# Optimization experiments

Hardware: AMD Instinct MI355X
Metric: run time of the kernel (lower is better)

The kernel has to match this reference:

```python
import jax, jax.numpy as jnp
import numpy as np

B, N, D, K = 8, 2048, 512, 16


def setup_inputs() -> dict:
    key = jax.random.key(0)
    k1, k2, k3, k4, k5 = jax.random.split(key, 5)
    s = 1.0 / np.sqrt(D)
    return {
        "x": jax.random.normal(k1, (B, N, D), dtype=jnp.float32),
        "attn_w": jax.random.uniform(k2, (K, D), jnp.float32, -s, s),
        "attn_b": jax.random.uniform(k3, (K,), jnp.float32, -s, s),
        "w_merged": jax.random.uniform(k4, (D, D), jnp.float32, -s, s),
        "w_orig": jax.random.uniform(k5, (D, D), jnp.float32, -s, s),
    }


def reference(x, attn_w, attn_b, w_merged, w_orig):
    b, n, d = x.shape
    k = attn_w.shape[0]
    # cosine similarity matrix [B,N,N]
    xn = x / jnp.linalg.norm(x, axis=2, keepdims=True)
    w = jnp.einsum('bnd,bmd->bnm', xn, xn)
    # top-k neighbours per row
    _, idx = jax.lax.top_k(w, k)  # [B,N,K]
    bi = jnp.arange(b)[:, None, None]
    ni = jnp.arange(n)[None, :, None]
    # scatter 1s at top-k positions, then symmetrize (mutual-knn mask)
    mask = jnp.zeros((b, n, n), x.dtype).at[bi, ni, idx].set(1.0)
    mask = mask * jnp.swapaxes(mask, 1, 2)
    # learned per-neighbour attention logits scattered into dense [B,N,N]
    attn = x @ attn_w.T + attn_b  # [B,N,K]
    attn_full = jnp.zeros((b, n, n), x.dtype).at[bi, ni, idx].set(attn)
    scores = attn_full * mask + (-1e9) * (1.0 - mask)
    adj = jax.nn.softmax(scores, axis=2)
    # weighted aggregation + two projections
    merged = jnp.einsum('bnm,bmd->bnd', adj, x)
    out = jax.nn.relu(merged @ w_merged.T) + x @ w_orig.T
    return out
```

## Files before the change

kernel.cpp:

```cpp
#include <hip/hip_runtime.h>
#include <math.h>


#define NTOK 2048
#define DIM 512

typedef __attribute__((ext_vector_type(8))) __bf16 bf16x8;
typedef __attribute__((ext_vector_type(4))) float f32x4;
typedef __attribute__((ext_vector_type(8))) unsigned short ushort8;

#define GLDS(gp, lp)                                                      \
  __builtin_amdgcn_global_load_lds(                                       \
      (const __attribute__((address_space(1))) void*)(gp),                \
      (__attribute__((address_space(3))) void*)(lp), 16, 0, 0)

__device__ __forceinline__ ushort f2b(float f) {
  unsigned u = __float_as_uint(f);
  return (ushort)((u + 0x7fffu + ((u >> 16) & 1u)) >> 16);
}
__device__ __forceinline__ float b2f(ushort h) {
  return __uint_as_float((unsigned)h << 16);
}
__device__ __forceinline__ ushort f2key(float v) {
  union { _Float16 h; ushort u; } cv;
  cv.h = (_Float16)v;
  ushort hb = cv.u;
  return (hb & 0x8000u) ? (ushort)~hb : (ushort)(hb | 0x8000u);
}

__global__ __launch_bounds__(64) void k_norm(const float* __restrict__ x,
                                             const float* __restrict__ aw,
                                             const float* __restrict__ ab,
                                             ushort* __restrict__ xnb,
                                             ushort* __restrict__ xb,
                                             double* __restrict__ inv64,
                                             float* __restrict__ L) {
  int row = blockIdx.x, lane = threadIdx.x;
  const float* xr = x + (size_t)row * DIM;
  float4 a = *(const float4*)&xr[lane * 8];
  float4 b = *(const float4*)&xr[lane * 8 + 4];

  float s[16];
#pragma unroll
  for (int k = 0; k < 16; ++k) {
    const float4 w0 = *(const float4*)&aw[(size_t)k * DIM + lane * 8];
    const float4 w1 = *(const float4*)&aw[(size_t)k * DIM + lane * 8 + 4];
    s[k] = a.x * w0.x + a.y * w0.y + a.z * w0.z + a.w * w0.w + b.x * w1.x +
           b.y * w1.y + b.z * w1.z + b.w * w1.w;
  }
#pragma unroll
  for (int off = 1; off < 64; off <<= 1)
#pragma unroll
    for (int k = 0; k < 16; ++k) s[k] += __shfl_xor(s[k], off);

  double ss = (double)a.x * a.x + (double)a.y * a.y + (double)a.z * a.z +
              (double)a.w * a.w + (double)b.x * b.x + (double)b.y * b.y +
              (double)b.z * b.z + (double)b.w * b.w;
#pragma unroll
  for (int off = 32; off >= 1; off >>= 1) ss += __shfl_xor(ss, off);
  double inv = 1.0 / sqrt(ss);
  if (lane == 0) {
    inv64[row] = inv;
#pragma unroll
    for (int k = 0; k < 16; ++k) L[(size_t)row * 16 + k] = s[k] + ab[k];
  }
  float f = (float)inv;
  size_t o = (size_t)row * DIM + lane * 8;
  ushort4 r0 = {f2b(a.x), f2b(a.y), f2b(a.z), f2b(a.w)};
  ushort4 r1 = {f2b(b.x), f2b(b.y), f2b(b.z), f2b(b.w)};
  *(ushort4*)&xb[o] = r0;
  *(ushort4*)&xb[o + 4] = r1;
  ushort4 n0 = {f2b(a.x * f), f2b(a.y * f), f2b(a.z * f), f2b(a.w * f)};
  ushort4 n1 = {f2b(b.x * f), f2b(b.y * f), f2b(b.z * f), f2b(b.w * f)};
  *(ushort4*)&xnb[o] = n0;
  *(ushort4*)&xnb[o + 4] = n1;
}

__global__ __launch_bounds__(256) void k_castw(const float* __restrict__ a,
                                               const float* __restrict__ b,
                                               ushort* __restrict__ ab,
                                               ushort* __restrict__ bb) {
  int i = (blockIdx.x * 256 + threadIdx.x) * 4;
  float4 va = *(const float4*)&a[i];
  float4 vb = *(const float4*)&b[i];
  ushort4 oa = {f2b(va.x), f2b(va.y), f2b(va.z), f2b(va.w)};
  ushort4 ob = {f2b(vb.x), f2b(vb.y), f2b(vb.z), f2b(vb.w)};
  *(ushort4*)&ab[i] = oa;
  *(ushort4*)&bb[i] = ob;
}

__device__ __forceinline__ void stage2(const ushort* __restrict__ A,
                                       const ushort* __restrict__ B,
                                       ushort* lA, ushort* lB, int rb, int cb,
                                       int kt, int wv, int ln) {
#pragma unroll
  for (int j = 0; j < 2; ++j) {
    int c = j * 256 + wv * 64 + ln;
    int r = c >> 2, seg = c & 3;
    GLDS(A + (size_t)(rb + r) * DIM + kt + seg * 8, lA + c * 8);
    GLDS(B + (size_t)(cb + r) * DIM + kt + seg * 8, lB + c * 8);
  }
}

__device__ __forceinline__ void frag_mfma(const ushort* lA, const ushort* lB,
                                          int wm, int wn, int col, int quad,
                                          f32x4 (&acc)[4][4]) {
  bf16x8 af[4], bf[4];
#pragma unroll
  for (int i = 0; i < 4; ++i) {
    af[i] = *(const bf16x8*)&lA[(wm * 64 + i * 16 + col) * 32 + quad * 8];
    bf[i] = *(const bf16x8*)&lB[(wn * 64 + i * 16 + col) * 32 + quad * 8];
  }
#pragma unroll
  for (int i = 0; i < 4; ++i)
#pragma unroll
    for (int j = 0; j < 4; ++j)
      acc[i][j] =
          __builtin_amdgcn_mfma_f32_16x16x32_bf16(af[i], bf[j], acc[i][j], 0, 0, 0);
}

__global__ __launch_bounds__(256) void k_simgemm(const ushort* __restrict__ Xn,
                                                 ushort* __restrict__ Skey) {
  __shared__ __align__(16) ushort lA0[128 * 32];
  __shared__ __align__(16) ushort lB0[128 * 32];
  __shared__ __align__(16) ushort st[128 * 136];
  ushort* lA1 = st;
  ushort* lB1 = st + 128 * 32;
  int tid = threadIdx.x;
  int z = blockIdx.z;
  const ushort* Xb = Xn + (size_t)z * NTOK * DIM;
  ushort* Sb = Skey + (size_t)z * NTOK * NTOK;
  int ti = 0, rem = blockIdx.x;
  while (rem >= 16 - ti) { rem -= 16 - ti; ++ti; }
  int tj = ti + rem;
  int rb = ti * 128, cb = tj * 128;
  int wv = tid >> 6, ln = tid & 63;
  int wm = wv >> 1, wn = wv & 1;
  int col = ln & 15, quad = ln >> 4;
  f32x4 zero = {0.f, 0.f, 0.f, 0.f};
  f32x4 acc[4][4];
#pragma unroll
  for (int i = 0; i < 4; ++i)
#pragma unroll
    for (int j = 0; j < 4; ++j) acc[i][j] = zero;

  stage2(Xb, Xb, lA0, lB0, rb, cb, 0, wv, ln);
  __syncthreads();
#pragma unroll
  for (int kt16 = 0; kt16 < 16; ++kt16) {
    const ushort* cA = (kt16 & 1) ? lA1 : lA0;
    const ushort* cB = (kt16 & 1) ? lB1 : lB0;
    if (kt16 < 15)
      stage2(Xb, Xb, (kt16 & 1) ? lA0 : lA1, (kt16 & 1) ? lB0 : lB1, rb, cb,
             (kt16 + 1) * 32, wv, ln);
    frag_mfma(cA, cB, wm, wn, col, quad, acc);
    __syncthreads();
  }

#pragma unroll
  for (int i = 0; i < 4; ++i)
#pragma unroll
    for (int j = 0; j < 4; ++j) {
      int r0 = wm * 64 + i * 16 + quad * 4;
      int c = wn * 64 + j * 16 + col;
      ushort4 kk = {f2key(acc[i][j][0]), f2key(acc[i][j][1]),
                    f2key(acc[i][j][2]), f2key(acc[i][j][3])};
      *(ushort4*)&Sb[(size_t)(cb + c) * NTOK + rb + r0] = kk;
      st[(r0 + 0) * 136 + c] = kk.x;
      st[(r0 + 1) * 136 + c] = kk.y;
      st[(r0 + 2) * 136 + c] = kk.z;
      st[(r0 + 3) * 136 + c] = kk.w;
    }
  __syncthreads();
#pragma unroll
  for (int p = 0; p < 8; ++p) {
    int r = p * 16 + (tid >> 4);
    int cs = (tid & 15) * 8;
    ushort8 row = *(const ushort8*)&st[r * 136 + cs];
    *(ushort8*)&Sb[(size_t)(rb + r) * NTOK + cb + cs] = row;
  }
}

__global__ __launch_bounds__(256) void k_proj(const ushort* __restrict__ Mg,
                                              const ushort* __restrict__ Wm,
                                              const ushort* __restrict__ Xg,
                                              const ushort* __restrict__ Wo,
                                              float* __restrict__ out) {
  __shared__ __align__(16) ushort lds[32768];
  ushort* A1a = lds;
  ushort* B1a = lds + 4096;
  ushort* A2a = lds + 8192;
  ushort* B2a = lds + 12288;
  ushort* A1b = lds + 16384;
  ushort* B1b = lds + 20480;
  ushort* A2b = lds + 24576;
  ushort* B2b = lds + 28672;
  int tid = threadIdx.x;
  int rb = blockIdx.x * 128, cb = blockIdx.y * 128;
  int wv = tid >> 6, ln = tid & 63;
  int wm = wv >> 1, wn = wv & 1;
  int col = ln & 15, quad = ln >> 4;
  f32x4 zero = {0.f, 0.f, 0.f, 0.f};
  f32x4 a1[4][4], a2[4][4];
#pragma unroll
  for (int i = 0; i < 4; ++i)
#pragma unroll
    for (int j = 0; j < 4; ++j) { a1[i][j] = zero; a2[i][j] = zero; }

  stage2(Mg, Wm, A1a, B1a, rb, cb, 0, wv, ln);
  stage2(Xg, Wo, A2a, B2a, rb, cb, 0, wv, ln);
  __syncthreads();
#pragma unroll
  for (int kt16 = 0; kt16 < 16; ++kt16) {
    const bool odd = kt16 & 1;
    const ushort* cA1 = odd ? A1b : A1a;
    const ushort* cB1 = odd ? B1b : B1a;
    const ushort* cA2 = odd ? A2b : A2a;
    const ushort* cB2 = odd ? B2b : B2a;
    if (kt16 < 15) {
      stage2(Mg, Wm, odd ? A1a : A1b, odd ? B1a : B1b, rb, cb,
             (kt16 + 1) * 32, wv, ln);
      stage2(Xg, Wo, odd ? A2a : A2b, odd ? B2a : B2b, rb, cb,
             (kt16 + 1) * 32, wv, ln);
    }
    frag_mfma(cA1, cB1, wm, wn, col, quad, a1);
    frag_mfma(cA2, cB2, wm, wn, col, quad, a2);
    __syncthreads();
  }

#pragma unroll
  for (int i = 0; i < 4; ++i)
#pragma unroll
    for (int j = 0; j < 4; ++j)
#pragma unroll
      for (int r = 0; r < 4; ++r) {
        int m = rb + wm * 64 + i * 16 + quad * 4 + r;
        int n = cb + wn * 64 + j * 16 + col;
        out[(size_t)m * DIM + n] = fmaxf(a1[i][j][r], 0.f) + a2[i][j][r];
      }
}

#define TARGET 24

__device__ __forceinline__ void scan_pick(const unsigned* hist, int lane,
                                          int tgt, int* out_v,
                                          unsigned* out_cntv1) {
  int base = lane * 4;
  unsigned h0 = hist[0 * 256 + base + 0] + hist[1 * 256 + base + 0] +
                hist[2 * 256 + base + 0] + hist[3 * 256 + base + 0];
  unsigned h1 = hist[0 * 256 + base + 1] + hist[1 * 256 + base + 1] +
                hist[2 * 256 + base + 1] + hist[3 * 256 + base + 1];
  unsigned h2 = hist[0 * 256 + base + 2] + hist[1 * 256 + base + 2] +
                hist[2 * 256 + base + 2] + hist[3 * 256 + base + 2];
  unsigned h3 = hist[0 * 256 + base + 3] + hist[1 * 256 + base + 3] +
                hist[2 * 256 + base + 3] + hist[3 * 256 + base + 3];
  unsigned s3 = h3, s2 = h2 + s3, s1 = h1 + s2, s0 = h0 + s1;
  unsigned inc = s0;
#pragma unroll
  for (int off = 1; off < 64; off <<= 1) {
    unsigned o = __shfl_down(inc, off);
    if (lane + off < 64) inc += o;
  }
  unsigned above = inc - s0;
  int vb = -1;
  if (above + s0 >= (unsigned)tgt) vb = base + 0;
  if (above + s1 >= (unsigned)tgt) vb = base + 1;
  if (above + s2 >= (unsigned)tgt) vb = base + 2;
  if (above + s3 >= (unsigned)tgt) vb = base + 3;
  int v = vb;
#pragma unroll
  for (int off = 1; off < 64; off <<= 1) v = max(v, __shfl_xor(v, off));
  unsigned v1 = 0;
  if ((v >> 2) == lane) {
    int k = v & 3;
    v1 = (k == 0) ? above + s1 : (k == 1) ? above + s2
                               : (k == 2) ? above + s3 : above;
  }
  v1 = __shfl(v1, v >> 2);
  *out_v = v;
  *out_cntv1 = v1;
}

__global__ __launch_bounds__(256) void k_topk(const ushort* __restrict__ simk,
                                              const float* __restrict__ x,
                                              const double* __restrict__ inv64,
                                              int* __restrict__ idx16,
                                              int batch0, int pbm1, int pbsh) {
  int zi = blockIdx.x & pbm1;
  int n = blockIdx.x >> pbsh;
  int batch = batch0 + zi;
  int t = threadIdx.x;
  int wave = t >> 6, lane = t & 63;
  __shared__ unsigned hist[4 * 256];
  __shared__ int lidx[32];
  __shared__ double vals[32];
  __shared__ int shv, sneed, sthr, lcnt;
  const ushort* srow = simk + ((size_t)zi * NTOK + (size_t)n) * NTOK;

  const float* xrow = x + ((size_t)batch * NTOK + n) * DIM;
  float4 xa0 = *(const float4*)&xrow[lane * 8];
  float4 xa1 = *(const float4*)&xrow[lane * 8 + 4];
  double dinvn = inv64[(size_t)batch * NTOK + n];

  ushort kv[8];
  {
    ushort8 v8 = *(const ushort8*)&srow[t * 8];
#pragma unroll
    for (int e = 0; e < 8; ++e) kv[e] = v8[e];
  }
#pragma unroll
  for (int i = 0; i < 4; ++i) hist[t + 256 * i] = 0;
  if (t == 0) lcnt = 0;
  __syncthreads();
#pragma unroll
  for (int j = 0; j < 8; ++j)
    atomicAdd(&hist[wave * 256 + (kv[j] >> 8)], 1u);
  __syncthreads();
  if (wave == 0) {
    int v;
    unsigned v1;
    scan_pick(hist, lane, TARGET, &v, &v1);
    if (lane == 0) { shv = v; sneed = TARGET - (int)v1; }
  }
  __syncthreads();
  int v = shv;
#pragma unroll
  for (int i = 0; i < 4; ++i) hist[t + 256 * i] = 0;
  __syncthreads();
#pragma unroll
  for (int j = 0; j < 8; ++j)
    if ((kv[j] >> 8) == v) atomicAdd(&hist[wave * 256 + (kv[j] & 255)], 1u);
  __syncthreads();
  if (wave == 0) {
    int u;
    unsigned dummy;
    scan_pick(hist, lane, sneed, &u, &dummy);
    if (lane == 0) sthr = (v << 8) | u;
  }
  __syncthreads();
  unsigned thr = (unsigned)sthr;
#pragma unroll
  for (int j = 0; j < 8; ++j) {
    if ((unsigned)kv[j] >= thr) {
      int slot = atomicAdd(&lcnt, 1);
      if (slot < 32) lidx[slot] = t * 8 + j;
    }
  }
  __syncthreads();
  int c = lcnt < 32 ? lcnt : 32;
  for (int s = wave; s < c; s += 4) {
    int m = lidx[s];
    const float* xc = x + ((size_t)batch * NTOK + m) * DIM;
    float4 b0 = *(const float4*)&xc[lane * 8];
    float4 b1 = *(const float4*)&xc[lane * 8 + 4];
    double sacc = 0.0;
    sacc = fma((double)xa0.x, (double)b0.x, sacc);
    sacc = fma((double)xa0.y, (double)b0.y, sacc);
    sacc = fma((double)xa0.z, (double)b0.z, sacc);
    sacc = fma((double)xa0.w, (double)b0.w, sacc);
    sacc = fma((double)xa1.x, (double)b1.x, sacc);
    sacc = fma((double)xa1.y, (double)b1.y, sacc);
    sacc = fma((double)xa1.z, (double)b1.z, sacc);
    sacc = fma((double)xa1.w, (double)b1.w, sacc);
#pragma unroll
    for (int off = 1; off < 64; off <<= 1) sacc += __shfl_xor(sacc, off);
    if (lane == 0)
      vals[s] = sacc * dinvn * inv64[(size_t)batch * NTOK + m];
  }
  __syncthreads();
  if (t < 32) {
    double sv = (t < c) ? vals[t] : -1.0e300;
    int si = (t < c) ? lidx[t] : 0x7FFFFFFF;
#pragma unroll
    for (int k = 2; k <= 32; k <<= 1) {
#pragma unroll
      for (int jj = k >> 1; jj > 0; jj >>= 1) {
        double ov = __shfl_xor(sv, jj);
        int oi = __shfl_xor(si, jj);
        bool lower = (t & jj) == 0;
        bool desc = (t & k) == 0;
        bool takeFirst = (lower == desc);
        bool otherFirst = (ov > sv) || (ov == sv && oi < si);
        if (takeFirst == otherFirst) { sv = ov; si = oi; }
      }
    }
    if (t < 16) idx16[((size_t)batch * NTOK + n) * 16 + t] = si;
  }
}

__global__ __launch_bounds__(128) void k_merge(const ushort* __restrict__ xb,
                                               const int* __restrict__ idx16,
                                               const float* __restrict__ L,
                                               ushort* __restrict__ mergedb) {
  int b = blockIdx.x & 7;
  int n = blockIdx.x >> 3;
  int row = (b << 11) | n;
  int t = threadIdx.x;
  __shared__ float ps[16];
  __shared__ int ms[16];
  if (t < 64) {
    int k = t & 15;
    int m = idx16[(size_t)row * 16 + k];
    const int* mrow = idx16 + (size_t)(b * NTOK + m) * 16;
    int4 q0 = *(const int4*)&mrow[0];
    int4 q1 = *(const int4*)&mrow[4];
    int4 q2 = *(const int4*)&mrow[8];
    int4 q3 = *(const int4*)&mrow[12];
    bool mut = (q0.x == n) | (q0.y == n) | (q0.z == n) | (q0.w == n) |
               (q1.x == n) | (q1.y == n) | (q1.z == n) | (q1.w == n) |
               (q2.x == n) | (q2.y == n) | (q2.z == n) | (q2.w == n) |
               (q3.x == n) | (q3.y == n) | (q3.z == n) | (q3.w == n);
    float l = mut ? L[(size_t)row * 16 + k] : -__builtin_inff();
    float mx = l;
#pragma unroll
    for (int off = 1; off < 16; off <<= 1) mx = fmaxf(mx, __shfl_xor(mx, off));
    float e = mut ? __expf(l - mx) : 0.0f;
    float den = e;
#pragma unroll
    for (int off = 1; off < 16; off <<= 1) den += __shfl_xor(den, off);
    if (t < 16) { ps[t] = e / den; ms[t] = m; }
  }
  __syncthreads();
  float4 acc = {0.f, 0.f, 0.f, 0.f};
#pragma unroll
  for (int k = 0; k < 16; ++k) {
    float pk = ps[k];
    if (pk != 0.0f) {
      ushort4 v = *(const ushort4*)&xb[(size_t)(b * NTOK + ms[k]) * DIM + t * 4];
      acc.x = fmaf(pk, b2f(v.x), acc.x);
      acc.y = fmaf(pk, b2f(v.y), acc.y);
      acc.z = fmaf(pk, b2f(v.z), acc.z);
      acc.w = fmaf(pk, b2f(v.w), acc.w);
    }
  }
  ushort4 o = {f2b(acc.x), f2b(acc.y), f2b(acc.z), f2b(acc.w)};
  *(ushort4*)&mergedb[(size_t)row * DIM + t * 4] = o;
}

extern "C" void kernel_launch(void* const* d_in, const int* in_sizes, int n_in,
                              void* d_out, int out_size, void* d_ws,
                              size_t ws_size, hipStream_t stream) {
  const float* x = (const float*)d_in[0];
  const float* attn_w = (const float*)d_in[1];
  const float* attn_b = (const float*)d_in[2];
  const float* w_merged = (const float*)d_in[3];
  const float* w_orig = (const float*)d_in[4];
  float* out = (float*)d_out;

  char* w = (char*)d_ws;
  ushort* xnb = (ushort*)(w);
  ushort* xb = (ushort*)(w + 16777216);
  double* inv64 = (double*)(w + 33554432);
  ushort* wmb = (ushort*)(w + 33685504);
  ushort* wob = (ushort*)(w + 34209792);
  int* idx16 = (int*)(w + 34734080);
  float* L = (float*)(w + 35782656);
  ushort* simk = (ushort*)(w + 36831232);
  ushort* mergedb = (ushort*)(w + 36831232);

  size_t fixed = 36831232ull, per = 8388608ull;
  int pb = 1, pbsh = 0;
  if (ws_size >= fixed + 8 * per) { pb = 8; pbsh = 3; }
  else if (ws_size >= fixed + 4 * per) { pb = 4; pbsh = 2; }
  else if (ws_size >= fixed + 2 * per) { pb = 2; pbsh = 1; }

  k_norm<<<16384, 64, 0, stream>>>(x, attn_w, attn_b, xnb, xb, inv64, L);
  k_castw<<<256, 256, 0, stream>>>(w_merged, w_orig, wmb, wob);
  for (int b = 0; b < 8; b += pb) {
    k_simgemm<<<dim3(136, 1, pb), 256, 0, stream>>>(
        xnb + (size_t)b * NTOK * DIM, simk);
    k_topk<<<NTOK * pb, 256, 0, stream>>>(simk, x, inv64, idx16, b, pb - 1,
                                          pbsh);
  }
  k_merge<<<16384, 128, 0, stream>>>(xb, idx16, L, mergedb);
  k_proj<<<dim3(128, 4), 256, 0, stream>>>(mergedb, wmb, xb, wob, out);
}
```

Baseline: 301.1 us.

## Run top-k selection with one wavefront per row, dropping block barriers

Rewrites the per-row top-k kernel to use a single 64-lane wavefront instead of four. Each lane now holds 32 keys, builds one shared histogram instead of four per-wave ones, and replaces the atomic candidate compaction with a ballot/popcount prefix. This removes the __syncthreads barriers and the cross-wave histogram reduction. In exchange each row gets less parallelism, the exact rescoring loop runs serially on one wave, and the code relies on wave-synchronous LDS ordering with no explicit barriers.

```diff
diff --git a/kernel.cpp b/kernel.cpp
--- a/kernel.cpp
+++ b/kernel.cpp
@@ -245,16 +245,8 @@
 __device__ __forceinline__ void scan_pick(const unsigned* hist, int lane,
                                           int tgt, int* out_v,
                                           unsigned* out_cntv1) {
-  int base = lane * 4;
-  unsigned h0 = hist[0 * 256 + base + 0] + hist[1 * 256 + base + 0] +
-                hist[2 * 256 + base + 0] + hist[3 * 256 + base + 0];
-  unsigned h1 = hist[0 * 256 + base + 1] + hist[1 * 256 + base + 1] +
-                hist[2 * 256 + base + 1] + hist[3 * 256 + base + 1];
-  unsigned h2 = hist[0 * 256 + base + 2] + hist[1 * 256 + base + 2] +
-                hist[2 * 256 + base + 2] + hist[3 * 256 + base + 2];
-  unsigned h3 = hist[0 * 256 + base + 3] + hist[1 * 256 + base + 3] +
-                hist[2 * 256 + base + 3] + hist[3 * 256 + base + 3];
-  unsigned s3 = h3, s2 = h2 + s3, s1 = h1 + s2, s0 = h0 + s1;
+  uint4 h = *(const uint4*)&hist[lane * 4];
+  unsigned s3 = h.w, s2 = h.z + s3, s1 = h.y + s2, s0 = h.x + s1;
   unsigned inc = s0;
 #pragma unroll
   for (int off = 1; off < 64; off <<= 1) {
@@ -262,6 +254,7 @@
     if (lane + off < 64) inc += o;
   }
   unsigned above = inc - s0;
+  int base = lane * 4;
   int vb = -1;
   if (above + s0 >= (unsigned)tgt) vb = base + 0;
   if (above + s1 >= (unsigned)tgt) vb = base + 1;
@@ -281,74 +274,68 @@
   *out_cntv1 = v1;
 }
 
-__global__ __launch_bounds__(256) void k_topk(const ushort* __restrict__ simk,
-                                              const float* __restrict__ x,
-                                              const double* __restrict__ inv64,
-                                              int* __restrict__ idx16,
-                                              int batch0, int pbm1, int pbsh) {
+__global__ __launch_bounds__(64) void k_topk(const ushort* __restrict__ simk,
+                                             const float* __restrict__ x,
+                                             const double* __restrict__ inv64,
+                                             int* __restrict__ idx16,
+                                             int batch0, int pbm1, int pbsh) {
   int zi = blockIdx.x & pbm1;
   int n = blockIdx.x >> pbsh;
   int batch = batch0 + zi;
-  int t = threadIdx.x;
-  int wave = t >> 6, lane = t & 63;
-  __shared__ unsigned hist[4 * 256];
+  int lane = threadIdx.x;
+  __shared__ __align__(16) unsigned hist1[256];
+  __shared__ __align__(16) unsigned hist2[256];
   __shared__ int lidx[32];
   __shared__ double vals[32];
-  __shared__ int shv, sneed, sthr, lcnt;
   const ushort* srow = simk + ((size_t)zi * NTOK + (size_t)n) * NTOK;
-
   const float* xrow = x + ((size_t)batch * NTOK + n) * DIM;
+
   float4 xa0 = *(const float4*)&xrow[lane * 8];
   float4 xa1 = *(const float4*)&xrow[lane * 8 + 4];
   double dinvn = inv64[(size_t)batch * NTOK + n];
 
-  ushort kv[8];
-  {
-    ushort8 v8 = *(const ushort8*)&srow[t * 8];
-#pragma unroll
-    for (int e = 0; e < 8; ++e) kv[e] = v8[e];
-  }
-#pragma unroll
-  for (int i = 0; i < 4; ++i) hist[t + 256 * i] = 0;
-  if (t == 0) lcnt = 0;
-  __syncthreads();
-#pragma unroll
-  for (int j = 0; j < 8; ++j)
-    atomicAdd(&hist[wave * 256 + (kv[j] >> 8)], 1u);
-  __syncthreads();
-  if (wave == 0) {
-    int v;
-    unsigned v1;
-    scan_pick(hist, lane, TARGET, &v, &v1);
-    if (lane == 0) { shv = v; sneed = TARGET - (int)v1; }
-  }
-  __syncthreads();
-  int v = shv;
-#pragma unroll
-  for (int i = 0; i < 4; ++i) hist[t + 256 * i] = 0;
-  __syncthreads();
-#pragma unroll
-  for (int j = 0; j < 8; ++j)
-    if ((kv[j] >> 8) == v) atomicAdd(&hist[wave * 256 + (kv[j] & 255)], 1u);
-  __syncthreads();
-  if (wave == 0) {
-    int u;
-    unsigned dummy;
-    scan_pick(hist, lane, sneed, &u, &dummy);
-    if (lane == 0) sthr = (v << 8) | u;
-  }
-  __syncthreads();
-  unsigned thr = (unsigned)sthr;
-#pragma unroll
-  for (int j = 0; j < 8; ++j) {
-    if ((unsigned)kv[j] >= thr) {
-      int slot = atomicAdd(&lcnt, 1);
-      if (slot < 32) lidx[slot] = t * 8 + j;
+  ushort8 kk[4];
+#pragma unroll
+  for (int r = 0; r < 4; ++r)
+    kk[r] = *(const ushort8*)&srow[(r * 64 + lane) * 8];
+  hist1[lane] = 0; hist1[lane + 64] = 0;
+  hist1[lane + 128] = 0; hist1[lane + 192] = 0;
+  hist2[lane] = 0; hist2[lane + 64] = 0;
+  hist2[lane + 128] = 0; hist2[lane + 192] = 0;
+#pragma unroll
+  for (int r = 0; r < 4; ++r)
+#pragma unroll
+    for (int j = 0; j < 8; ++j)
+      atomicAdd(&hist1[kk[r][j] >> 8], 1u);
+  int v;
+  unsigned v1;
+  scan_pick(hist1, lane, TARGET, &v, &v1);
+  int need = TARGET - (int)v1;
+#pragma unroll
+  for (int r = 0; r < 4; ++r)
+#pragma unroll
+    for (int j = 0; j < 8; ++j)
+      if ((kk[r][j] >> 8) == v) atomicAdd(&hist2[kk[r][j] & 255], 1u);
+  int u;
+  unsigned dummy;
+  scan_pick(hist2, lane, need, &u, &dummy);
+  unsigned thr = (unsigned)((v << 8) | u);
+  int cnt = 0;
+  unsigned long long ltmask = (1ull << lane) - 1ull;
+#pragma unroll
+  for (int r = 0; r < 4; ++r)
+#pragma unroll
+    for (int j = 0; j < 8; ++j) {
+      bool p = (unsigned)kk[r][j] >= thr;
+      unsigned long long m = __ballot(p);
+      if (p) {
+        int pos = cnt + __popcll(m & ltmask);
+        if (pos < 32) lidx[pos] = (r * 64 + lane) * 8 + j;
+      }
+      cnt += __popcll(m);
     }
-  }
-  __syncthreads();
-  int c = lcnt < 32 ? lcnt : 32;
-  for (int s = wave; s < c; s += 4) {
+  int c = cnt < 32 ? cnt : 32;
+  for (int s = 0; s < c; ++s) {
     int m = lidx[s];
     const float* xc = x + ((size_t)batch * NTOK + m) * DIM;
     float4 b0 = *(const float4*)&xc[lane * 8];
@@ -367,24 +354,23 @@
     if (lane == 0)
       vals[s] = sacc * dinvn * inv64[(size_t)batch * NTOK + m];
   }
-  __syncthreads();
-  if (t < 32) {
-    double sv = (t < c) ? vals[t] : -1.0e300;
-    int si = (t < c) ? lidx[t] : 0x7FFFFFFF;
+  if (lane < 32) {
+    double sv = (lane < c) ? vals[lane] : -1.0e300;
+    int si = (lane < c) ? lidx[lane] : 0x7FFFFFFF;
 #pragma unroll
     for (int k = 2; k <= 32; k <<= 1) {
 #pragma unroll
       for (int jj = k >> 1; jj > 0; jj >>= 1) {
         double ov = __shfl_xor(sv, jj);
         int oi = __shfl_xor(si, jj);
-        bool lower = (t & jj) == 0;
-        bool desc = (t & k) == 0;
+        bool lower = (lane & jj) == 0;
+        bool desc = (lane & k) == 0;
         bool takeFirst = (lower == desc);
         bool otherFirst = (ov > sv) || (ov == sv && oi < si);
         if (takeFirst == otherFirst) { sv = ov; si = oi; }
       }
     }
-    if (t < 16) idx16[((size_t)batch * NTOK + n) * 16 + t] = si;
+    if (lane < 16) idx16[((size_t)batch * NTOK + n) * 16 + lane] = si;
   }
 }
 
@@ -469,8 +455,8 @@
   for (int b = 0; b < 8; b += pb) {
     k_simgemm<<<dim3(136, 1, pb), 256, 0, stream>>>(
         xnb + (size_t)b * NTOK * DIM, simk);
-    k_topk<<<NTOK * pb, 256, 0, stream>>>(simk, x, inv64, idx16, b, pb - 1,
-                                          pbsh);
+    k_topk<<<NTOK * pb, 64, 0, stream>>>(simk, x, inv64, idx16, b, pb - 1,
+                                         pbsh);
   }
   k_merge<<<16384, 128, 0, stream>>>(xb, idx16, L, mergedb);
   k_proj<<<dim3(128, 4), 256, 0, stream>>>(mergedb, wmb, xb, wob, out);
```

After: 287.0 us. 4.7% less time.
